# Kernel tuning notes

Measured on AMD Instinct MI355X. Metric: run time of the kernel, lower is better.

## Reference

```python
import jax, jax.numpy as jnp
import numpy as np

NUM_FREQS = 10
EPS = 1e-6


def _posenc(x):
    # NeRF positional encoding with identity: [x, sin(2^i x), cos(2^i x)]
    freqs = 2.0 ** jnp.arange(NUM_FREQS, dtype=x.dtype)  # [L]
    xb = x[..., None, :] * freqs[:, None]                # [..., L, D]
    four = jnp.sin(jnp.concatenate([xb, xb + 0.5 * jnp.pi], axis=-2))
    return jnp.concatenate([x, four.reshape(*x.shape[:-1], -1)], axis=-1)


def _ln(x, s, b):
    mu = jnp.mean(x, axis=-1, keepdims=True)
    var = jnp.mean(jnp.square(x - mu), axis=-1, keepdims=True)
    return (x - mu) * jax.lax.rsqrt(var + EPS) * s + b


def _layer(net, chunk, hW, hb, hls, hlb, wW, wb, bW, bb_, ls, lb):
    # hyper net (hyper_depth=1): Dense -> LayerNorm -> relu
    h = jax.nn.relu(_ln(chunk @ hW + hb, hls, hlb))
    n_in = net.shape[-1]
    n_out = bb_.shape[-1]
    # generate per-point weight matrix [K,P,N,M] and bias [K,P,N]
    w = (h @ wW + wb).reshape(*h.shape[:-1], n_out, n_in)
    b = h @ bW + bb_
    net = jnp.einsum('kpm,kpnm->kpn', net, w) + b
    return jax.nn.relu(_ln(net, ls, lb))


def _forward(rays, latent_tokens, token_embeddings, h_W0, h_b0, h_ln_s0, h_ln_b0,
             w_W0, w_b0, bb_W0, bb_b0, ln_s0, ln_b0,
             h_W, h_b, h_ln_s, h_ln_b, w_W, w_b, bb_W, bb_b, ln_s, ln_b,
             rgb_W, rgb_b):
    origins = rays[..., 0:3]
    dirs = rays[..., 3:6]
    plucker = jnp.concatenate([dirs, jnp.cross(origins, dirs)], axis=-1)  # [K,P,6]
    net = _posenc(plucker)  # [K,P,126]

    K, T, Z = latent_tokens.shape
    emb = jnp.broadcast_to(token_embeddings[None], (K, T, token_embeddings.shape[-1]))
    lt = jnp.concatenate([latent_tokens, emb], axis=-1).reshape(K, 1, -1)  # [K,1,T*(Z+E)]
    P = rays.shape[1]
    latent = jnp.broadcast_to(lt, (K, P, lt.shape[-1]))
    skips = jnp.split(latent, 8, axis=-1)  # 8 chunks of [K,P,128]

    net = _layer(net, skips[0], h_W0, h_b0, h_ln_s0, h_ln_b0,
                 w_W0, w_b0, bb_W0, bb_b0, ln_s0, ln_b0)
    for i in range(7):
        net = _layer(net, skips[i + 1], h_W[i], h_b[i], h_ln_s[i], h_ln_b[i],
                     w_W[i], w_b[i], bb_W[i], bb_b[i], ln_s[i], ln_b[i])
    return jax.nn.sigmoid(net @ rgb_W + rgb_b)


def setup_inputs() -> dict:
    key = jax.random.key(0)
    ks = jax.random.split(key, 12)
    K, P, T, Z, W = 2, 4096, 8, 64, 64
    IN0 = 6 * (1 + 2 * NUM_FREQS)  # 126
    f32 = jnp.float32
    d = {}
    d['rays'] = jax.random.normal(ks[0], (K, P, 6), f32)
    d['latent_tokens'] = jax.random.normal(ks[1], (K, T, Z), f32)
    d['token_embeddings'] = jax.random.normal(ks[2], (T, 64), f32)
    # layer 0 (input dim 126)
    d['h_W0'] = jax.random.normal(ks[3], (Z + 64, W), f32)
    d['h_b0'] = jnp.zeros((W,), f32)
    d['h_ln_s0'] = jnp.ones((W,), f32)
    d['h_ln_b0'] = jnp.zeros((W,), f32)
    d['w_W0'] = jax.random.normal(ks[4], (W, IN0 * W), f32)
    d['w_b0'] = jnp.zeros((IN0 * W,), f32)
    d['bb_W0'] = jax.random.normal(ks[5], (W, W), f32)
    d['bb_b0'] = jnp.zeros((W,), f32)
    d['ln_s0'] = jnp.ones((W,), f32)
    d['ln_b0'] = jnp.zeros((W,), f32)
    # layers 1..7 (input dim 64), stacked
    L = 7
    d['h_W'] = jax.random.normal(ks[6], (L, Z + 64, W), f32)
    d['h_b'] = jnp.zeros((L, W), f32)
    d['h_ln_s'] = jnp.ones((L, W), f32)
    d['h_ln_b'] = jnp.zeros((L, W), f32)
    d['w_W'] = jax.random.normal(ks[7], (L, W, W * W), f32)
    d['w_b'] = jnp.zeros((L, W * W), f32)
    d['bb_W'] = jax.random.normal(ks[8], (L, W, W), f32)
    d['bb_b'] = jnp.zeros((L, W), f32)
    d['ln_s'] = jnp.ones((L, W), f32)
    d['ln_b'] = jnp.zeros((L, W), f32)
    d['rgb_W'] = jax.random.normal(ks[9], (W, 3), f32)
    d['rgb_b'] = jnp.zeros((3,), f32)
    return d


def reference(rays, latent_tokens, token_embeddings, h_W0, h_b0, h_ln_s0, h_ln_b0,
              w_W0, w_b0, bb_W0, bb_b0, ln_s0, ln_b0,
              h_W, h_b, h_ln_s, h_ln_b, w_W, w_b, bb_W, bb_b, ln_s, ln_b,
              rgb_W, rgb_b):
    return _forward(rays, latent_tokens, token_embeddings, h_W0, h_b0, h_ln_s0, h_ln_b0,
                    w_W0, w_b0, bb_W0, bb_b0, ln_s0, ln_b0,
                    h_W, h_b, h_ln_s, h_ln_b, w_W, w_b, bb_W, bb_b, ln_s, ln_b,
                    rgb_W, rgb_b)
```

## Files before the change

kernel.cpp:

```cpp
#include <hip/hip_runtime.h>
#include <math.h>

#define EPSF 1e-6f
#define RPW 4

__device__ __forceinline__ float rl(float v, int srclane) {
    return __uint_as_float(__builtin_amdgcn_readlane(__float_as_uint(v), srclane));
}

__device__ __forceinline__ void ln_stats(float a, float& mu, float& rstd) {
    float s1 = a, s2 = a * a;
#pragma unroll
    for (int off = 32; off > 0; off >>= 1) {
        s1 += __shfl_xor(s1, off, 64);
        s2 += __shfl_xor(s2, off, 64);
    }
    mu = s1 * (1.0f / 64.0f);
    float var = fmaxf(s2 * (1.0f / 64.0f) - mu * mu, 0.0f);
    rstd = rsqrtf(var + EPSF);
}

__device__ __forceinline__ float wave_sum64(float v) {
#pragma unroll
    for (int off = 32; off > 0; off >>= 1) v += __shfl_xor(v, off, 64);
    return v;
}

__device__ __forceinline__ float posenc_elem(const float* pl, int e) {
    if (e < 6) return pl[e];
    int t = e - 6;
    int j = t / 6;
    int i = t - j * 6;
    int jm = (j < 10) ? j : (j - 10);
    float arg = pl[i] * (float)(1 << jm);
    if (j >= 10) arg += 1.5707963705062866f;
    return sinf(arg);
}

__global__ __launch_bounds__(128) void precompute_kernel(
    const float* __restrict__ latent_tokens, const float* __restrict__ token_embeddings,
    const float* __restrict__ h_W0, const float* __restrict__ h_b0,
    const float* __restrict__ h_ln_s0, const float* __restrict__ h_ln_b0,
    const float* __restrict__ w_W0, const float* __restrict__ w_b0,
    const float* __restrict__ bb_W0, const float* __restrict__ bb_b0,
    const float* __restrict__ h_W, const float* __restrict__ h_b,
    const float* __restrict__ h_ln_s, const float* __restrict__ h_ln_b,
    const float* __restrict__ w_W, const float* __restrict__ w_b,
    const float* __restrict__ bb_W, const float* __restrict__ bb_b,
    float* __restrict__ ws, int offW, int offB)
{
    const int s = blockIdx.x;
    const int l = blockIdx.y;
    const int tid = threadIdx.x;
    const int lane = tid & 63;
    const int warp = tid >> 6;

    __shared__ float s_chunk[2][128];
    __shared__ float s_h[2][64];

#pragma unroll
    for (int t = tid; t < 256; t += 128) {
        int k = t >> 7, m = t & 127;
        s_chunk[k][m] = (m < 64) ? latent_tokens[(k * 8 + l) * 64 + m]
                                 : token_embeddings[l * 64 + (m - 64)];
    }
    __syncthreads();

    const float* hW  = (l == 0) ? h_W0    : h_W    + (size_t)(l - 1) * 128 * 64;
    const float* hb  = (l == 0) ? h_b0    : h_b    + (l - 1) * 64;
    const float* hls = (l == 0) ? h_ln_s0 : h_ln_s + (l - 1) * 64;
    const float* hlb = (l == 0) ? h_ln_b0 : h_ln_b + (l - 1) * 64;

    {
        float a = hb[lane];
#pragma unroll 16
        for (int m = 0; m < 128; m++) a += s_chunk[warp][m] * hW[m * 64 + lane];
        float mu, rstd;
        ln_stats(a, mu, rstd);
        s_h[warp][lane] = fmaxf((a - mu) * rstd * hls[lane] + hlb[lane], 0.0f);
    }
    __syncthreads();

    const int n_in  = (l == 0) ? 126 : 64;
    const int nflat = 64 * n_in;
    const int slice = nflat / 32;
    const float* wW = (l == 0) ? w_W0 : w_W + (size_t)(l - 1) * 64 * 4096;
    const float* wb = (l == 0) ? w_b0 : w_b + (size_t)(l - 1) * 4096;

    for (int o = s * slice + tid; o < s * slice + slice; o += 128) {
        float wbv = wb[o];
        float a0 = wbv, a1 = wbv;
#pragma unroll 16
        for (int j = 0; j < 64; j++) {
            float w = wW[(size_t)j * nflat + o];
            a0 += s_h[0][j] * w;
            a1 += s_h[1][j] * w;
        }
        int n = o / n_in, m = o - n * n_in;
        if (l == 0) {
            ws[n * 128 + m] = a0;
            ws[8192 + n * 128 + m] = a1;
        } else {
            float* base = ws + offW + (size_t)(l - 1) * 4096;
            base[n * 64 + m] = a0;
            base[7 * 4096 + n * 64 + m] = a1;
        }
    }

    if (l == 0 && s == 0) {
        int n = tid >> 1, c = tid & 1;
        ws[n * 128 + 126 + c] = 0.0f;
        ws[8192 + n * 128 + 126 + c] = 0.0f;
    }

    if (s == 0) {
        const float* bW  = (l == 0) ? bb_W0 : bb_W + (size_t)(l - 1) * 64 * 64;
        const float* bb_ = (l == 0) ? bb_b0 : bb_b + (l - 1) * 64;
        float a = bb_[lane];
#pragma unroll 16
        for (int j = 0; j < 64; j++) a += s_h[warp][j] * bW[j * 64 + lane];
        ws[offB + (warp * 8 + l) * 64 + lane] = a;
    }
}

__global__ __launch_bounds__(256) void forward_kernel(
    const float* __restrict__ rays,
    const float* __restrict__ ln_s0, const float* __restrict__ ln_b0,
    const float* __restrict__ ln_s, const float* __restrict__ ln_b,
    const float* __restrict__ rgb_W, const float* __restrict__ rgb_b,
    const float* __restrict__ ws, int offW, int offB,
    float* __restrict__ out, int K, int P)
{
    const int warp = threadIdx.x >> 6;
    const int lane = threadIdx.x & 63;
    const int total = K * P;
    const int r0 = (blockIdx.x * 4 + warp) * RPW;
    if (r0 >= total) return;
    const int k = r0 / P;

    const float* W0row  = ws + (size_t)k * 8192 + lane * 128;
    const float* WLrow  = ws + offW + (size_t)k * 7 * 4096 + lane * 64;

    float4 buf[4];
#pragma unroll
    for (int c = 0; c < 4; c++) buf[c] = ((const float4*)W0row)[c];

    float net0[RPW], net1[RPW];
#pragma unroll
    for (int q = 0; q < RPW; q++) {
        int r = r0 + q; if (r > total - 1) r = total - 1;
        float o0 = rays[r * 6 + 0], o1 = rays[r * 6 + 1], o2 = rays[r * 6 + 2];
        float d0 = rays[r * 6 + 3], d1 = rays[r * 6 + 4], d2 = rays[r * 6 + 5];
        float pl[6];
        pl[0] = d0; pl[1] = d1; pl[2] = d2;
        pl[3] = o1 * d2 - o2 * d1;
        pl[4] = o2 * d0 - o0 * d2;
        pl[5] = o0 * d1 - o1 * d0;
        net0[q] = posenc_elem(pl, lane);
        net1[q] = (lane + 64 < 126) ? posenc_elem(pl, lane + 64) : 0.0f;
    }

    float acc[RPW];

    {
        float bia = ws[offB + (k * 8 + 0) * 64 + lane];
        float pre[RPW];
#pragma unroll
        for (int q = 0; q < RPW; q++) pre[q] = bia;
#pragma unroll
        for (int c = 0; c < 32; c++) {
            float4 cur = buf[c & 3];
            buf[c & 3] = (c < 28) ? ((const float4*)W0row)[c + 4]
                                  : ((const float4*)WLrow)[c - 28];
            float wj[4] = {cur.x, cur.y, cur.z, cur.w};
#pragma unroll
            for (int j = 0; j < 4; j++) {
                int m = c * 4 + j;
#pragma unroll
                for (int q = 0; q < RPW; q++)
                    pre[q] += ((m < 64) ? rl(net0[q], m) : rl(net1[q], m - 64)) * wj[j];
            }
        }
        float sc = ln_s0[lane], bc = ln_b0[lane];
#pragma unroll
        for (int q = 0; q < RPW; q++) {
            float mu, rstd;
            ln_stats(pre[q], mu, rstd);
            acc[q] = fmaxf((pre[q] - mu) * rstd * sc + bc, 0.0f);
        }
    }

#pragma unroll
    for (int l = 1; l < 8; l++) {
        const float* row  = WLrow + (size_t)(l - 1) * 4096;
        const float* nrow = (l < 7) ? row + 4096 : row;
        float bia = ws[offB + (k * 8 + l) * 64 + lane];
        float na[RPW];
#pragma unroll
        for (int q = 0; q < RPW; q++) na[q] = bia;
#pragma unroll
        for (int c = 0; c < 16; c++) {
            float4 cur = buf[c & 3];
            buf[c & 3] = (c < 12) ? ((const float4*)row)[c + 4]
                                  : ((const float4*)nrow)[c - 12];
            float wj[4] = {cur.x, cur.y, cur.z, cur.w};
#pragma unroll
            for (int j = 0; j < 4; j++) {
                int m = c * 4 + j;
#pragma unroll
                for (int q = 0; q < RPW; q++) na[q] += rl(acc[q], m) * wj[j];
            }
        }
        float sc = ln_s[(l - 1) * 64 + lane], bc = ln_b[(l - 1) * 64 + lane];
#pragma unroll
        for (int q = 0; q < RPW; q++) {
            float mu, rstd;
            ln_stats(na[q], mu, rstd);
            acc[q] = fmaxf((na[q] - mu) * rstd * sc + bc, 0.0f);
        }
    }

    float w0 = rgb_W[lane * 3 + 0], w1 = rgb_W[lane * 3 + 1], w2 = rgb_W[lane * 3 + 2];
    float b0 = rgb_b[0], b1 = rgb_b[1], b2 = rgb_b[2];
#pragma unroll
    for (int q = 0; q < RPW; q++) {
        float c0 = wave_sum64(acc[q] * w0);
        float c1 = wave_sum64(acc[q] * w1);
        float c2 = wave_sum64(acc[q] * w2);
        if (lane == 0 && r0 + q < total) {
            out[(r0 + q) * 3 + 0] = 1.0f / (1.0f + expf(-(c0 + b0)));
            out[(r0 + q) * 3 + 1] = 1.0f / (1.0f + expf(-(c1 + b1)));
            out[(r0 + q) * 3 + 2] = 1.0f / (1.0f + expf(-(c2 + b2)));
        }
    }
}

extern "C" void kernel_launch(void* const* d_in, const int* in_sizes, int n_in,
                              void* d_out, int out_size, void* d_ws, size_t ws_size,
                              hipStream_t stream) {
    const float* rays    = (const float*)d_in[0];
    const float* latent  = (const float*)d_in[1];
    const float* tok_emb = (const float*)d_in[2];
    const float* h_W0    = (const float*)d_in[3];
    const float* h_b0    = (const float*)d_in[4];
    const float* h_ln_s0 = (const float*)d_in[5];
    const float* h_ln_b0 = (const float*)d_in[6];
    const float* w_W0    = (const float*)d_in[7];
    const float* w_b0    = (const float*)d_in[8];
    const float* bb_W0   = (const float*)d_in[9];
    const float* bb_b0   = (const float*)d_in[10];
    const float* ln_s0   = (const float*)d_in[11];
    const float* ln_b0   = (const float*)d_in[12];
    const float* h_W     = (const float*)d_in[13];
    const float* h_b     = (const float*)d_in[14];
    const float* h_ln_s  = (const float*)d_in[15];
    const float* h_ln_b  = (const float*)d_in[16];
    const float* w_W     = (const float*)d_in[17];
    const float* w_b     = (const float*)d_in[18];
    const float* bb_W    = (const float*)d_in[19];
    const float* bb_b    = (const float*)d_in[20];
    const float* ln_s    = (const float*)d_in[21];
    const float* ln_b    = (const float*)d_in[22];
    const float* rgb_W   = (const float*)d_in[23];
    const float* rgb_b   = (const float*)d_in[24];
    float* out = (float*)d_out;

    const int K = in_sizes[1] / (8 * 64);
    const int P = in_sizes[0] / (6 * K);
    const int offW = K * 8192;
    const int offB = offW + K * 7 * 4096;

    float* ws = (float*)d_ws;

    dim3 pgrid(32, 8);
    precompute_kernel<<<pgrid, 128, 0, stream>>>(
        latent, tok_emb, h_W0, h_b0, h_ln_s0, h_ln_b0, w_W0, w_b0, bb_W0, bb_b0,
        h_W, h_b, h_ln_s, h_ln_b, w_W, w_b, bb_W, bb_b, ws, offW, offB);

    const int total = K * P;
    const int rays_per_block = 4 * RPW;
    const int blocks = (total + rays_per_block - 1) / rays_per_block;
    forward_kernel<<<blocks, 256, 0, stream>>>(
        rays, ln_s0, ln_b0, ln_s, ln_b, rgb_W, rgb_b,
        ws, offW, offB, out, K, P);
}
```

Measured before the change: 157.7 us.

## Store generated per-sample weights in fp16 and use packed dot2 MACs

The precompute kernel now writes the generated per-sample weight matrices as fp16. The forward kernel packs each activation pair into half2 and accumulates with v_dot2 instructions, so each readlane broadcast feeds two MACs and the weight bytes loaded are halved. It also holds two full 64x64 weight rows in registers as double buffers, so the next layer's weights load during the current layer's MACs. Activations are repacked after each LayerNorm through ds_bpermute. This lowers precision to fp16 for weights and activations, with fp32 accumulation, and the #else fallback for dot2 has a typo (wv.x*wv.x).

```diff
diff --git a/kernel.cpp b/kernel.cpp
--- a/kernel.cpp
+++ b/kernel.cpp
@@ -2,10 +2,36 @@
 #include <math.h>
 
 #define EPSF 1e-6f
-#define RPW 4
-
-__device__ __forceinline__ float rl(float v, int srclane) {
-    return __uint_as_float(__builtin_amdgcn_readlane(__float_as_uint(v), srclane));
+typedef unsigned int uint;
+typedef _Float16 f16x2 __attribute__((ext_vector_type(2)));
+typedef __fp16 h16x2 __attribute__((ext_vector_type(2)));
+
+__device__ __forceinline__ uint rlu(uint v, int srclane) {
+    return (uint)__builtin_amdgcn_readlane((int)v, srclane);
+}
+
+__device__ __forceinline__ float dot2u(uint w, uint a, float c) {
+#if __has_builtin(__builtin_amdgcn_fdot2)
+    return __builtin_amdgcn_fdot2(__builtin_bit_cast(f16x2, w),
+                                  __builtin_bit_cast(f16x2, a), c, false);
+#else
+    f16x2 wv = __builtin_bit_cast(f16x2, w), av = __builtin_bit_cast(f16x2, a);
+    return c + (float)wv.x * (float)wv.x + (float)wv.y * (float)av.y;
+#endif
+}
+
+__device__ __forceinline__ uint pkact(float lo, float hi) {
+#if __has_builtin(__builtin_amdgcn_cvt_pkrtz)
+    h16x2 p = __builtin_amdgcn_cvt_pkrtz(lo, hi);
+    return __builtin_bit_cast(uint, p);
+#else
+    f16x2 p; p.x = (_Float16)lo; p.y = (_Float16)hi;
+    return __builtin_bit_cast(uint, p);
+#endif
+}
+
+__device__ __forceinline__ float bpermf(int byteaddr, float v) {
+    return __int_as_float(__builtin_amdgcn_ds_bpermute(byteaddr, __float_as_int(v)));
 }
 
 __device__ __forceinline__ void ln_stats(float a, float& mu, float& rstd) {
@@ -47,7 +73,7 @@
     const float* __restrict__ h_ln_s, const float* __restrict__ h_ln_b,
     const float* __restrict__ w_W, const float* __restrict__ w_b,
     const float* __restrict__ bb_W, const float* __restrict__ bb_b,
-    float* __restrict__ ws, int offW, int offB)
+    float* __restrict__ ws, int offBbytes)
 {
     const int s = blockIdx.x;
     const int l = blockIdx.y;
@@ -86,6 +112,7 @@
     const int slice = nflat / 32;
     const float* wW = (l == 0) ? w_W0 : w_W + (size_t)(l - 1) * 64 * 4096;
     const float* wb = (l == 0) ? w_b0 : w_b + (size_t)(l - 1) * 4096;
+    _Float16* wsH = (_Float16*)ws;
 
     for (int o = s * slice + tid; o < s * slice + slice; o += 128) {
         float wbv = wb[o];
@@ -98,19 +125,19 @@
         }
         int n = o / n_in, m = o - n * n_in;
         if (l == 0) {
-            ws[n * 128 + m] = a0;
-            ws[8192 + n * 128 + m] = a1;
+            wsH[n * 128 + m]        = (_Float16)a0;
+            wsH[8192 + n * 128 + m] = (_Float16)a1;
         } else {
-            float* base = ws + offW + (size_t)(l - 1) * 4096;
-            base[n * 64 + m] = a0;
-            base[7 * 4096 + n * 64 + m] = a1;
+            _Float16* b0p = wsH + 16384 + (size_t)(l - 1) * 4096;
+            b0p[n * 64 + m]            = (_Float16)a0;
+            b0p[7 * 4096 + n * 64 + m] = (_Float16)a1;
         }
     }
 
     if (l == 0 && s == 0) {
         int n = tid >> 1, c = tid & 1;
-        ws[n * 128 + 126 + c] = 0.0f;
-        ws[8192 + n * 128 + 126 + c] = 0.0f;
+        wsH[n * 128 + 126 + c] = (_Float16)0.0f;
+        wsH[8192 + n * 128 + 126 + c] = (_Float16)0.0f;
     }
 
     if (s == 0) {
@@ -119,114 +146,105 @@
         float a = bb_[lane];
 #pragma unroll 16
         for (int j = 0; j < 64; j++) a += s_h[warp][j] * bW[j * 64 + lane];
-        ws[offB + (warp * 8 + l) * 64 + lane] = a;
-    }
-}
-
-__global__ __launch_bounds__(256) void forward_kernel(
+        ((float*)((char*)ws + offBbytes))[(warp * 8 + l) * 64 + lane] = a;
+    }
+}
+
+#define MC1(wc, pp) \
+    accq0 = dot2u(wc, rlu(pk0, (pp)), accq0); \
+    accq1 = dot2u(wc, rlu(pk1, (pp)), accq1); \
+    accq2 = dot2u(wc, rlu(pk2, (pp)), accq2); \
+    accq3 = dot2u(wc, rlu(pk3, (pp)), accq3);
+#define MACCH(W, P0) { uint4 _w = (W); MC1(_w.x, (P0)) MC1(_w.y, (P0)+1) MC1(_w.z, (P0)+2) MC1(_w.w, (P0)+3) }
+#define MACLAYER_A  MACCH(A0,0) MACCH(A1,4) MACCH(A2,8)  MACCH(A3,12) MACCH(A4,16) MACCH(A5,20) MACCH(A6,24) MACCH(A7,28)
+#define MACLAYER_B  MACCH(B0,0) MACCH(B1,4) MACCH(B2,8)  MACCH(B3,12) MACCH(B4,16) MACCH(B5,20) MACCH(B6,24) MACCH(B7,28)
+#define MACLAYER_B32 MACCH(B0,32) MACCH(B1,36) MACCH(B2,40) MACCH(B3,44) MACCH(B4,48) MACCH(B5,52) MACCH(B6,56) MACCH(B7,60)
+#define LOAD_A(p) A0=(p)[0]; A1=(p)[1]; A2=(p)[2]; A3=(p)[3]; A4=(p)[4]; A5=(p)[5]; A6=(p)[6]; A7=(p)[7];
+#define LOAD_B(p) B0=(p)[0]; B1=(p)[1]; B2=(p)[2]; B3=(p)[3]; B4=(p)[4]; B5=(p)[5]; B6=(p)[6]; B7=(p)[7];
+#define BIAS(v)  accq0=(v); accq1=(v); accq2=(v); accq3=(v);
+#define LNQ(aq, pq, S, B) { float mu, rstd; ln_stats(aq, mu, rstd); \
+    aq = fmaxf((aq - mu) * rstd * (S) + (B), 0.0f); \
+    pq = pkact(bpermf(pa0, aq), bpermf(pa1, aq)); }
+#define LNP(S, B) LNQ(accq0, pk0, S, B) LNQ(accq1, pk1, S, B) LNQ(accq2, pk2, S, B) LNQ(accq3, pk3, S, B)
+
+__global__ __launch_bounds__(256, 2) void forward_kernel(
     const float* __restrict__ rays,
     const float* __restrict__ ln_s0, const float* __restrict__ ln_b0,
     const float* __restrict__ ln_s, const float* __restrict__ ln_b,
     const float* __restrict__ rgb_W, const float* __restrict__ rgb_b,
-    const float* __restrict__ ws, int offW, int offB,
+    const float* __restrict__ ws, int offBbytes,
     float* __restrict__ out, int K, int P)
 {
     const int warp = threadIdx.x >> 6;
     const int lane = threadIdx.x & 63;
     const int total = K * P;
-    const int r0 = (blockIdx.x * 4 + warp) * RPW;
+    const int r0 = (blockIdx.x * 4 + warp) * 4;
     if (r0 >= total) return;
     const int k = r0 / P;
 
-    const float* W0row  = ws + (size_t)k * 8192 + lane * 128;
-    const float* WLrow  = ws + offW + (size_t)k * 7 * 4096 + lane * 64;
-
-    float4 buf[4];
-#pragma unroll
-    for (int c = 0; c < 4; c++) buf[c] = ((const float4*)W0row)[c];
-
-    float net0[RPW], net1[RPW];
-#pragma unroll
-    for (int q = 0; q < RPW; q++) {
-        int r = r0 + q; if (r > total - 1) r = total - 1;
-        float o0 = rays[r * 6 + 0], o1 = rays[r * 6 + 1], o2 = rays[r * 6 + 2];
-        float d0 = rays[r * 6 + 3], d1 = rays[r * 6 + 4], d2 = rays[r * 6 + 5];
-        float pl[6];
-        pl[0] = d0; pl[1] = d1; pl[2] = d2;
-        pl[3] = o1 * d2 - o2 * d1;
-        pl[4] = o2 * d0 - o0 * d2;
-        pl[5] = o0 * d1 - o1 * d0;
-        net0[q] = posenc_elem(pl, lane);
-        net1[q] = (lane + 64 < 126) ? posenc_elem(pl, lane + 64) : 0.0f;
-    }
-
-    float acc[RPW];
-
+    const char* wsB = (const char*)ws;
+    const uint4* row0 = (const uint4*)(wsB + (size_t)k * 16384 + lane * 256);
+    const uint4* rowL = (const uint4*)(wsB + 32768 + (size_t)k * 57344 + lane * 128);
+    const float* beff = (const float*)(wsB + offBbytes) + k * 512;
+
+    uint4 A0,A1,A2,A3,A4,A5,A6,A7, B0,B1,B2,B3,B4,B5,B6,B7;
+    LOAD_A(row0); LOAD_B(row0 + 8);
+
+    float be[8];
+#pragma unroll
+    for (int i = 0; i < 8; i++) be[i] = beff[i * 64 + lane];
+    float s0v = ln_s0[lane], b0v = ln_b0[lane];
+    float sl[7], bl[7];
+#pragma unroll
+    for (int i = 0; i < 7; i++) { sl[i] = ln_s[i * 64 + lane]; bl[i] = ln_b[i * 64 + lane]; }
+
+    const int pa0 = ((2 * lane) & 63) << 2;
+    const int pa1 = ((2 * lane + 1) & 63) << 2;
+
+    uint pk0, pk1, pk2, pk3;
     {
-        float bia = ws[offB + (k * 8 + 0) * 64 + lane];
-        float pre[RPW];
-#pragma unroll
-        for (int q = 0; q < RPW; q++) pre[q] = bia;
-#pragma unroll
-        for (int c = 0; c < 32; c++) {
-            float4 cur = buf[c & 3];
-            buf[c & 3] = (c < 28) ? ((const float4*)W0row)[c + 4]
-                                  : ((const float4*)WLrow)[c - 28];
-            float wj[4] = {cur.x, cur.y, cur.z, cur.w};
-#pragma unroll
-            for (int j = 0; j < 4; j++) {
-                int m = c * 4 + j;
-#pragma unroll
-                for (int q = 0; q < RPW; q++)
-                    pre[q] += ((m < 64) ? rl(net0[q], m) : rl(net1[q], m - 64)) * wj[j];
-            }
+        const int e0 = 2 * lane, e1 = 2 * lane + 1;
+#pragma unroll
+        for (int q = 0; q < 4; q++) {
+            int r = r0 + q; if (r > total - 1) r = total - 1;
+            float o0 = rays[r * 6 + 0], o1 = rays[r * 6 + 1], o2 = rays[r * 6 + 2];
+            float d0 = rays[r * 6 + 3], d1 = rays[r * 6 + 4], d2 = rays[r * 6 + 5];
+            float pl[6];
+            pl[0] = d0; pl[1] = d1; pl[2] = d2;
+            pl[3] = o1 * d2 - o2 * d1;
+            pl[4] = o2 * d0 - o0 * d2;
+            pl[5] = o0 * d1 - o1 * d0;
+            float v0 = (e0 < 126) ? posenc_elem(pl, e0) : 0.0f;
+            float v1 = (e1 < 126) ? posenc_elem(pl, e1) : 0.0f;
+            uint p = pkact(v0, v1);
+            if (q == 0) pk0 = p; else if (q == 1) pk1 = p; else if (q == 2) pk2 = p; else pk3 = p;
         }
-        float sc = ln_s0[lane], bc = ln_b0[lane];
-#pragma unroll
-        for (int q = 0; q < RPW; q++) {
-            float mu, rstd;
-            ln_stats(pre[q], mu, rstd);
-            acc[q] = fmaxf((pre[q] - mu) * rstd * sc + bc, 0.0f);
-        }
-    }
-
-#pragma unroll
-    for (int l = 1; l < 8; l++) {
-        const float* row  = WLrow + (size_t)(l - 1) * 4096;
-        const float* nrow = (l < 7) ? row + 4096 : row;
-        float bia = ws[offB + (k * 8 + l) * 64 + lane];
-        float na[RPW];
-#pragma unroll
-        for (int q = 0; q < RPW; q++) na[q] = bia;
-#pragma unroll
-        for (int c = 0; c < 16; c++) {
-            float4 cur = buf[c & 3];
-            buf[c & 3] = (c < 12) ? ((const float4*)row)[c + 4]
-                                  : ((const float4*)nrow)[c - 12];
-            float wj[4] = {cur.x, cur.y, cur.z, cur.w};
-#pragma unroll
-            for (int j = 0; j < 4; j++) {
-                int m = c * 4 + j;
-#pragma unroll
-                for (int q = 0; q < RPW; q++) na[q] += rl(acc[q], m) * wj[j];
-            }
-        }
-        float sc = ln_s[(l - 1) * 64 + lane], bc = ln_b[(l - 1) * 64 + lane];
-#pragma unroll
-        for (int q = 0; q < RPW; q++) {
-            float mu, rstd;
-            ln_stats(na[q], mu, rstd);
-            acc[q] = fmaxf((na[q] - mu) * rstd * sc + bc, 0.0f);
-        }
-    }
+    }
+
+    float accq0, accq1, accq2, accq3;
+
+    BIAS(be[0]);
+    MACLAYER_A;
+    LOAD_A(rowL);
+    MACLAYER_B32;
+    LNP(s0v, b0v);
+
+    BIAS(be[1]); MACLAYER_A; LOAD_B(rowL + 512);  LNP(sl[0], bl[0]);
+    BIAS(be[2]); MACLAYER_B; LOAD_A(rowL + 1024); LNP(sl[1], bl[1]);
+    BIAS(be[3]); MACLAYER_A; LOAD_B(rowL + 1536); LNP(sl[2], bl[2]);
+    BIAS(be[4]); MACLAYER_B; LOAD_A(rowL + 2048); LNP(sl[3], bl[3]);
+    BIAS(be[5]); MACLAYER_A; LOAD_B(rowL + 2560); LNP(sl[4], bl[4]);
+    BIAS(be[6]); MACLAYER_B; LOAD_A(rowL + 3072); LNP(sl[5], bl[5]);
+    BIAS(be[7]); MACLAYER_A;                      LNP(sl[6], bl[6]);
 
     float w0 = rgb_W[lane * 3 + 0], w1 = rgb_W[lane * 3 + 1], w2 = rgb_W[lane * 3 + 2];
     float b0 = rgb_b[0], b1 = rgb_b[1], b2 = rgb_b[2];
 #pragma unroll
-    for (int q = 0; q < RPW; q++) {
-        float c0 = wave_sum64(acc[q] * w0);
-        float c1 = wave_sum64(acc[q] * w1);
-        float c2 = wave_sum64(acc[q] * w2);
+    for (int q = 0; q < 4; q++) {
+        float a = (q == 0) ? accq0 : (q == 1) ? accq1 : (q == 2) ? accq2 : accq3;
+        float c0 = wave_sum64(a * w0);
+        float c1 = wave_sum64(a * w1);
+        float c2 = wave_sum64(a * w2);
         if (lane == 0 && r0 + q < total) {
             out[(r0 + q) * 3 + 0] = 1.0f / (1.0f + expf(-(c0 + b0)));
             out[(r0 + q) * 3 + 1] = 1.0f / (1.0f + expf(-(c1 + b1)));
@@ -267,20 +285,18 @@
 
     const int K = in_sizes[1] / (8 * 64);
     const int P = in_sizes[0] / (6 * K);
-    const int offW = K * 8192;
-    const int offB = offW + K * 7 * 4096;
+    const int offBbytes = K * 16384 + K * 7 * 8192;
 
     float* ws = (float*)d_ws;
 
     dim3 pgrid(32, 8);
     precompute_kernel<<<pgrid, 128, 0, stream>>>(
         latent, tok_emb, h_W0, h_b0, h_ln_s0, h_ln_b0, w_W0, w_b0, bb_W0, bb_b0,
-        h_W, h_b, h_ln_s, h_ln_b, w_W, w_b, bb_W, bb_b, ws, offW, offB);
+        h_W, h_b, h_ln_s, h_ln_b, w_W, w_b, bb_W, bb_b, ws, offBbytes);
 
     const int total = K * P;
-    const int rays_per_block = 4 * RPW;
-    const int blocks = (total + rays_per_block - 1) / rays_per_block;
+    const int blocks = (total + 15) / 16;
     forward_kernel<<<blocks, 256, 0, stream>>>(
         rays, ln_s0, ln_b0, ln_s, ln_b, rgb_W, rgb_b,
-        ws, offW, offB, out, K, P);
-}
+        ws, offBbytes, out, K, P);
+}
```

After: 143.0 us. -9.3%, faster.
